# Kernel tuning notes

Hardware: AMD Instinct MI355X
Metric: run time of the kernel (lower is better)

## Reference

```python
import jax, jax.numpy as jnp
import numpy as np

B, T, D = 2, 2048, 1024
H, DH = 16, 64


def setup_inputs() -> dict:
    key = jax.random.key(0)
    ks = jax.random.split(key, 8)
    return {
        "x": jax.random.normal(ks[0], (B, T, D), dtype=jnp.float32),
        "mask": jnp.ones((1, 1, T, T), dtype=bool),
        "Wq": jax.random.normal(ks[1], (D, D), dtype=jnp.float32) * 0.02,
        "Wk": jax.random.normal(ks[2], (D, D), dtype=jnp.float32) * 0.02,
        "Wv": jax.random.normal(ks[3], (D, D), dtype=jnp.float32) * 0.02,
        "Wo": jax.random.normal(ks[4], (D, D), dtype=jnp.float32) * 0.02,
        "S_q": jax.random.normal(ks[5], (H, DH, DH), dtype=jnp.float32),
        "S_k": jax.random.normal(ks[6], (H, DH, DH), dtype=jnp.float32),
    }


def reference(x, mask, Wq, Wk, Wv, Wo, S_q, S_k):
    b, t, _ = x.shape
    scale = DH ** (-0.5)
    # nn.Linear applies x @ W.T; our Wq etc. are the Linear weight matrices.
    def split_heads(y):
        return y.reshape(b, t, H, DH).transpose(0, 2, 1, 3)  # (B,H,T,DH)

    Q = split_heads(x @ Wq.T)
    K = split_heads(x @ Wk.T)
    V = split_heads(x @ Wv.T)
    Qp = jnp.einsum('bhtd,hde->bhte', Q, S_q)
    Kp = jnp.einsum('bhtd,hde->bhte', K, S_k)
    scores = jnp.einsum('bhte,bhse->bhts', Qp, Kp) * scale  # (B,H,T,T)
    scores = jnp.where(mask, scores, -jnp.inf)
    attn = jax.nn.softmax(scores, axis=-1)
    out = jnp.einsum('bhts,bhsd->bhtd', attn, V)
    out = out.transpose(0, 2, 1, 3).reshape(b, t, D)
    return out @ Wo.T
```

## Files before the change

kernel.cpp:

```cpp
#include <hip/hip_runtime.h>
#include <cstdint>
#include <cmath>


#define B_   2
#define T_   2048
#define Dm   1024
#define H_   16
#define DH_  64
#define Ntok (B_ * T_)
#define ND   (Ntok * Dm)
#define DD   (Dm * Dm)
#define QKS  2048

typedef _Float16 f16;
typedef _Float16 f16x4 __attribute__((ext_vector_type(4)));
typedef _Float16 f16x8 __attribute__((ext_vector_type(8)));
typedef float    f32x4 __attribute__((ext_vector_type(4)));

__device__ inline f32x4 mfma16(f16x8 a, f16x8 b, f32x4 c) {
  return __builtin_amdgcn_mfma_f32_16x16x32_f16(a, b, c, 0, 0, 0);
}

__device__ inline void async16(const void* g, void* l) {
  __builtin_amdgcn_global_load_lds(
      (const __attribute__((address_space(1))) unsigned int*)g,
      (__attribute__((address_space(3))) unsigned int*)l, 16, 0, 0);
}

__device__ inline float vmax4(f32x4 v) {
  return fmaxf(fmaxf(v[0], v[1]), fmaxf(v[2], v[3]));
}
__device__ inline float vsum4(f32x4 v) {
  return (v[0] + v[1]) + (v[2] + v[3]);
}

__global__ void cvt_all(const float* __restrict__ x, const float* __restrict__ Wv,
                        const float* __restrict__ Wo, f16* __restrict__ x_f,
                        f16* __restrict__ WvDst, f16* __restrict__ Wo_f) {
  int i = (blockIdx.x * 256 + threadIdx.x) * 4;
  const float* src;
  f16* dst;
  int off;
  if (i < ND) {
    src = x; dst = x_f; off = i;
  } else if (i < ND + DD) {
    src = Wv; dst = WvDst; off = i - ND;
  } else {
    src = Wo; dst = Wo_f; off = i - ND - DD;
  }
  f32x4 v = *(const f32x4*)(src + off);
  f16x4 o;
#pragma unroll
  for (int j = 0; j < 4; ++j) o[j] = (f16)v[j];
  *(f16x4*)(dst + off) = o;
}

__global__ __launch_bounds__(64) void fold_w2(
    const float* __restrict__ Wq, const float* __restrict__ Sq,
    const float* __restrict__ Wk, const float* __restrict__ Sk,
    f16* __restrict__ T) {
  __shared__ __align__(16) float sS[64 * 64];
  const int tid = threadIdx.x;
  const int hy = blockIdx.y;
  const float* W = (hy < 16) ? Wq : Wk;
  const float* S = (hy < 16) ? Sq : Sk;
  f16* out = T + (size_t)((hy < 16) ? 0 : 1024) * Dm;
  const int h = hy & 15;
  const int d = blockIdx.x * 64 + tid;
#pragma unroll 8
  for (int i = 0; i < 64; ++i) sS[i * 64 + tid] = S[h * 4096 + i * 64 + tid];
  __syncthreads();
  float acc[64];
#pragma unroll
  for (int e = 0; e < 64; ++e) acc[e] = 0.f;
  for (int c = 0; c < 64; ++c) {
    float wv = W[(size_t)(h * 64 + c) * Dm + d];
    const f32x4* srow = (const f32x4*)&sS[c * 64];
#pragma unroll
    for (int e4 = 0; e4 < 16; ++e4) {
      f32x4 sv = srow[e4];
      acc[e4 * 4 + 0] += wv * sv[0];
      acc[e4 * 4 + 1] += wv * sv[1];
      acc[e4 * 4 + 2] += wv * sv[2];
      acc[e4 * 4 + 3] += wv * sv[3];
    }
  }
#pragma unroll
  for (int e = 0; e < 64; ++e)
    out[(size_t)(h * 64 + e) * Dm + d] = (f16)acc[e];
}

template <int OUTMODE, int TN>
__global__ __launch_bounds__(256) void gemm_bt(
    const f16* __restrict__ A, const f16* __restrict__ B,
    float* __restrict__ Cf, f16* __restrict__ Ch, f16* __restrict__ Ct,
    int M, int N, int K) {
  constexpr int AS = 128 * 32;
  constexpr int BS = TN * 32;
  constexpr int MT = (TN == 128) ? 4 : 2;
  extern __shared__ __align__(16) f16 smem[];

  const int tid = threadIdx.x;
  const int w = tid >> 6, lane = tid & 63, g = lane >> 4, ln = lane & 15;
  const int wm = (TN == 128) ? (w >> 1) * 64 : w * 32;
  const int wn = (TN == 128) ? (w & 1) * 64 : 0;
  const int bm = blockIdx.y * 128, bn = blockIdx.x * TN;

  f32x4 acc[MT][4] = {};
  const int r0 = tid >> 2;
  const int kb = (tid & 3) * 8;

  auto issue = [&](int kc, int buf) {
    f16* dA = smem + buf * AS;
    f16* dB = smem + 2 * AS + buf * BS;
#pragma unroll
    for (int i = 0; i < 2; ++i) {
      size_t aoff = (size_t)(bm + i * 64 + r0) * K + kc + kb;
      int lo = i * 4096 + w * 1024;
      async16(A + aoff, (char*)dA + lo);
      if (TN == 128 || i == 0) {
        size_t boff = (size_t)(bn + i * 64 + r0) * K + kc + kb;
        async16(B + boff, (char*)dB + lo);
      }
    }
  };

  issue(0, 0);
  const int KI = K / 32;
  for (int i = 0; i < KI; ++i) {
    __syncthreads();
    if (i + 1 < KI) issue((i + 1) * 32, (i + 1) & 1);
    const f16* cA = smem + (i & 1) * AS;
    const f16* cB = smem + 2 * AS + (i & 1) * BS;
    f16x8 af[MT];
#pragma unroll
    for (int mt = 0; mt < MT; ++mt)
      af[mt] = *(const f16x8*)&cA[(wm + mt * 16 + ln) * 32 + g * 8];
#pragma unroll
    for (int nt = 0; nt < 4; ++nt) {
      f16x8 bf = *(const f16x8*)&cB[(wn + nt * 16 + ln) * 32 + g * 8];
#pragma unroll
      for (int mt = 0; mt < MT; ++mt)
        acc[mt][nt] = mfma16(af[mt], bf, acc[mt][nt]);
    }
  }

  if (OUTMODE == 3 && bn >= 2048) {
#pragma unroll
    for (int mt = 0; mt < MT; ++mt)
#pragma unroll
      for (int nt = 0; nt < 4; ++nt) {
        int ch = bn - 2048 + wn + nt * 16 + ln;
        size_t base = (size_t)ch * Ntok + bm + wm + mt * 16 + g * 4;
        f16x4 ov;
#pragma unroll
        for (int r = 0; r < 4; ++r) ov[r] = (f16)acc[mt][nt][r];
        *(f16x4*)&Ct[base] = ov;
      }
    return;
  }
#pragma unroll
  for (int mt = 0; mt < MT; ++mt)
#pragma unroll
    for (int nt = 0; nt < 4; ++nt)
#pragma unroll
      for (int r = 0; r < 4; ++r) {
        int row = bm + wm + mt * 16 + g * 4 + r;
        int col = bn + wn + nt * 16 + ln;
        float v = acc[mt][nt][r];
        if (OUTMODE == 0) {
          Cf[(size_t)row * N + col] = v;
        } else {
          Ch[(size_t)row * QKS + col] = (f16)v;
        }
      }
}

__global__ __launch_bounds__(512) void flash_attn(
    const f16* __restrict__ QK, const f16* __restrict__ Vt,
    f16* __restrict__ O) {
  __shared__ __align__(16) f16 sKV[2 * 8192];
  __shared__ __align__(16) f16 sP[8 * 16 * 88];
  constexpr int VOFF = 4096;

  const int tid = threadIdx.x;
  const int w = tid >> 6, lane = tid & 63, g = lane >> 4, ln = lane & 15;
  const int bh = blockIdx.y, b = bh >> 4, h = bh & 15;
  const int q0 = blockIdx.x * 256 + w * 32;
  const size_t rowBase = (size_t)b * T_;
  const int hc = h * DH_;

  f16x8 qf[2][2];
#pragma unroll
  for (int t = 0; t < 2; ++t) {
    size_t qrow = (rowBase + q0 + t * 16 + ln) * (size_t)QKS + hc;
#pragma unroll
    for (int s = 0; s < 2; ++s)
      qf[t][s] = *(const f16x8*)(QK + qrow + s * 32 + g * 8);
  }

  float mrow[2] = {-INFINITY, -INFINITY}, lrow[2] = {0.f, 0.f};
  f32x4 oacc[2][4] = {};

  const int srow = tid >> 3;
  const int sel = ((tid & 7) * 8) ^ ((srow & 7) * 8);

  auto issue = [&](int kc, int buf) {
    char* base = (char*)sKV + buf * 16384;
    size_t koff = (rowBase + kc + srow) * (size_t)QKS + 1024 + hc + sel;
    async16(QK + koff, base + tid * 16);
    size_t voff = (size_t)(hc + srow) * Ntok + rowBase + kc + sel;
    async16(Vt + voff, base + 8192 + tid * 16);
  };

  issue(0, 0);
  constexpr int NC = T_ / 64;
  for (int i = 0; i < NC; ++i) {
    __syncthreads();
    if (i + 1 < NC) issue((i + 1) * 64, (i + 1) & 1);
    const f16* cK = sKV + (i & 1) * 8192;
    const f16* cVT = cK + VOFF;

    const int c0 = (g * 8) ^ ((ln & 7) * 8);
    const int c1 = (32 + g * 8) ^ ((ln & 7) * 8);

    f32x4 s4[2][4];
#pragma unroll
    for (int nt = 0; nt < 4; ++nt) {
      int row = (nt * 16 + ln) * 64;
      f16x8 k80 = *(const f16x8*)&cK[row + c0];
      f16x8 k81 = *(const f16x8*)&cK[row + c1];
#pragma unroll
      for (int t = 0; t < 2; ++t) {
        f32x4 a = {};
        a = mfma16(k80, qf[t][0], a);
        a = mfma16(k81, qf[t][1], a);
        s4[t][nt] = a * 0.1803368801111244f;
      }
    }

    f16* pw = sP + w * (16 * 88);
    f16x8 pb[2][2];
#pragma unroll
    for (int t = 0; t < 2; ++t) {
      f32x4 m4 = s4[t][0];
#pragma unroll
      for (int nt = 1; nt < 4; ++nt) {
        m4[0] = fmaxf(m4[0], s4[t][nt][0]);
        m4[1] = fmaxf(m4[1], s4[t][nt][1]);
        m4[2] = fmaxf(m4[2], s4[t][nt][2]);
        m4[3] = fmaxf(m4[3], s4[t][nt][3]);
      }
      float mx = vmax4(m4);
      mx = fmaxf(mx, __shfl_xor(mx, 16, 64));
      mx = fmaxf(mx, __shfl_xor(mx, 32, 64));
      float mn = fmaxf(mrow[t], mx);
      float alpha = __builtin_amdgcn_exp2f(mrow[t] - mn);
      mrow[t] = mn;
      f32x4 p4[4];
      f16x4 pk[4];
#pragma unroll
      for (int nt = 0; nt < 4; ++nt)
#pragma unroll
        for (int r = 0; r < 4; ++r) {
          float pv = __builtin_amdgcn_exp2f(s4[t][nt][r] - mn);
          p4[nt][r] = pv;
          pk[nt][r] = (f16)pv;
        }
      f32x4 sv4 = (p4[0] + p4[1]) + (p4[2] + p4[3]);
      float sum = vsum4(sv4);
      sum += __shfl_xor(sum, 16, 64);
      sum += __shfl_xor(sum, 32, 64);
      lrow[t] = lrow[t] * alpha + sum;
      if (__any(alpha != 1.0f)) {
#pragma unroll
        for (int dt = 0; dt < 4; ++dt) oacc[t][dt] *= alpha;
      }
#pragma unroll
      for (int nt = 0; nt < 4; ++nt)
        *(f16x4*)&pw[ln * 88 + nt * 16 + g * 4] = pk[nt];
      asm volatile("" ::: "memory");
#pragma unroll
      for (int s = 0; s < 2; ++s)
        pb[t][s] = *(const f16x8*)&pw[ln * 88 + s * 32 + g * 8];
      asm volatile("" ::: "memory");
    }

#pragma unroll
    for (int s = 0; s < 2; ++s) {
      int col = (s == 0) ? c0 : c1;
#pragma unroll
      for (int dt = 0; dt < 4; ++dt) {
        f16x8 va = *(const f16x8*)&cVT[(dt * 16 + ln) * 64 + col];
        oacc[0][dt] = mfma16(va, pb[0][s], oacc[0][dt]);
        oacc[1][dt] = mfma16(va, pb[1][s], oacc[1][dt]);
      }
    }
  }

#pragma unroll
  for (int t = 0; t < 2; ++t) {
    float rl = 1.0f / lrow[t];
    size_t orow = (rowBase + q0 + t * 16 + ln) * (size_t)Dm + hc;
#pragma unroll
    for (int dt = 0; dt < 4; ++dt) {
      f16x4 ov;
#pragma unroll
      for (int r = 0; r < 4; ++r) ov[r] = (f16)(oacc[t][dt][r] * rl);
      *(f16x4*)&O[orow + dt * 16 + g * 4] = ov;
    }
  }
}

extern "C" void kernel_launch(void* const* d_in, const int* in_sizes, int n_in,
                              void* d_out, int out_size, void* d_ws, size_t ws_size,
                              hipStream_t stream) {
  const float* x  = (const float*)d_in[0];
  const float* Wq = (const float*)d_in[2];
  const float* Wk = (const float*)d_in[3];
  const float* Wv = (const float*)d_in[4];
  const float* Wo = (const float*)d_in[5];
  const float* Sq = (const float*)d_in[6];
  const float* Sk = (const float*)d_in[7];

  char* p = (char*)d_ws;
  auto alloc = [&](size_t bytes) {
    char* r = p;
    p += (bytes + 255) & ~(size_t)255;
    return r;
  };
  f16* x_f   = (f16*)alloc((size_t)ND * 2);
  f16* Wqkv  = (f16*)alloc((size_t)3 * DD * 2);
  f16* Wo_f  = (f16*)alloc((size_t)DD * 2);
  f16* QK    = (f16*)alloc((size_t)Ntok * QKS * 2);
  f16* Vt_f  = (f16*)alloc((size_t)ND * 2);
  f16* AO    = (f16*)alloc((size_t)ND * 2);

  cvt_all<<<(ND + 2 * DD) / 1024, 256, 0, stream>>>(
      x, Wv, Wo, x_f, Wqkv + (size_t)2048 * Dm, Wo_f);
  fold_w2<<<dim3(16, 32), 64, 0, stream>>>(Wq, Sq, Wk, Sk, Wqkv);

  gemm_bt<3, 128><<<dim3(3072 / 128, Ntok / 128), 256, 32768, stream>>>(
      x_f, Wqkv, nullptr, QK, Vt_f, Ntok, 3072, Dm);

  flash_attn<<<dim3(T_ / 256, B_ * H_), 512, 0, stream>>>(QK, Vt_f, AO);

  gemm_bt<0, 64><<<dim3(Dm / 64, Ntok / 128), 256, 24576, stream>>>(
      AO, Wo_f, (float*)d_out, nullptr, nullptr, Ntok, Dm, Dm);
}
```

Before: 236.9 us.

## Split flash attention over two KV halves and merge with combine kernel

```diff
diff --git a/kernel.cpp b/kernel.cpp
--- a/kernel.cpp
+++ b/kernel.cpp
@@ -179,7 +179,7 @@
 
 __global__ __launch_bounds__(512) void flash_attn(
     const f16* __restrict__ QK, const f16* __restrict__ Vt,
-    f16* __restrict__ O) {
+    f16* __restrict__ Op, float* __restrict__ Mp, float* __restrict__ Lp) {
   __shared__ __align__(16) f16 sKV[2 * 8192];
   __shared__ __align__(16) f16 sP[8 * 16 * 88];
   constexpr int VOFF = 4096;
@@ -187,6 +187,8 @@
   const int tid = threadIdx.x;
   const int w = tid >> 6, lane = tid & 63, g = lane >> 4, ln = lane & 15;
   const int bh = blockIdx.y, b = bh >> 4, h = bh & 15;
+  const int sp = blockIdx.z;
+  const int kbase = sp * (T_ / 2);
   const int q0 = blockIdx.x * 256 + w * 32;
   const size_t rowBase = (size_t)b * T_;
   const int hc = h * DH_;
@@ -196,8 +198,12 @@
   for (int t = 0; t < 2; ++t) {
     size_t qrow = (rowBase + q0 + t * 16 + ln) * (size_t)QKS + hc;
 #pragma unroll
-    for (int s = 0; s < 2; ++s)
-      qf[t][s] = *(const f16x8*)(QK + qrow + s * 32 + g * 8);
+    for (int s = 0; s < 2; ++s) {
+      f16x8 q = *(const f16x8*)(QK + qrow + s * 32 + g * 8);
+#pragma unroll
+      for (int j = 0; j < 8; ++j) q[j] *= (f16)0.1803368801111244f;
+      qf[t][s] = q;
+    }
   }
 
   float mrow[2] = {-INFINITY, -INFINITY}, lrow[2] = {0.f, 0.f};
@@ -214,11 +220,11 @@
     async16(Vt + voff, base + 8192 + tid * 16);
   };
 
-  issue(0, 0);
-  constexpr int NC = T_ / 64;
+  issue(kbase, 0);
+  constexpr int NC = T_ / 2 / 64;
   for (int i = 0; i < NC; ++i) {
     __syncthreads();
-    if (i + 1 < NC) issue((i + 1) * 64, (i + 1) & 1);
+    if (i + 1 < NC) issue(kbase + (i + 1) * 64, (i + 1) & 1);
     const f16* cK = sKV + (i & 1) * 8192;
     const f16* cVT = cK + VOFF;
 
@@ -236,7 +242,7 @@
         f32x4 a = {};
         a = mfma16(k80, qf[t][0], a);
         a = mfma16(k81, qf[t][1], a);
-        s4[t][nt] = a * 0.1803368801111244f;
+        s4[t][nt] = a;
       }
     }
 
@@ -301,16 +307,47 @@
 
 #pragma unroll
   for (int t = 0; t < 2; ++t) {
-    float rl = 1.0f / lrow[t];
-    size_t orow = (rowBase + q0 + t * 16 + ln) * (size_t)Dm + hc;
+    size_t q = rowBase + q0 + t * 16 + ln;
+    size_t orow = ((size_t)sp * Ntok + q) * Dm + hc;
 #pragma unroll
     for (int dt = 0; dt < 4; ++dt) {
       f16x4 ov;
 #pragma unroll
-      for (int r = 0; r < 4; ++r) ov[r] = (f16)(oacc[t][dt][r] * rl);
-      *(f16x4*)&O[orow + dt * 16 + g * 4] = ov;
-    }
-  }
+      for (int r = 0; r < 4; ++r) ov[r] = (f16)oacc[t][dt][r];
+      *(f16x4*)&Op[orow + dt * 16 + g * 4] = ov;
+    }
+    if (g == 0) {
+      Mp[((size_t)sp * Ntok + q) * H_ + h] = mrow[t];
+      Lp[((size_t)sp * Ntok + q) * H_ + h] = lrow[t];
+    }
+  }
+}
+
+__global__ void flash_combine(const f16* __restrict__ Op,
+                              const float* __restrict__ Mp,
+                              const float* __restrict__ Lp,
+                              f16* __restrict__ AO) {
+  int idx = blockIdx.x * 256 + threadIdx.x;
+  int tok = idx >> 8;
+  int c4 = idx & 255;
+  int ch = c4 * 4;
+  int h = ch >> 6;
+  float m0 = Mp[(size_t)tok * H_ + h];
+  float m1 = Mp[((size_t)Ntok + tok) * H_ + h];
+  float l0 = Lp[(size_t)tok * H_ + h];
+  float l1 = Lp[((size_t)Ntok + tok) * H_ + h];
+  float mM = fmaxf(m0, m1);
+  float a0 = __builtin_amdgcn_exp2f(m0 - mM);
+  float a1 = __builtin_amdgcn_exp2f(m1 - mM);
+  float rl = 1.0f / (a0 * l0 + a1 * l1);
+  a0 *= rl;
+  a1 *= rl;
+  f16x4 o0 = *(const f16x4*)&Op[(size_t)tok * Dm + ch];
+  f16x4 o1 = *(const f16x4*)&Op[((size_t)Ntok + tok) * Dm + ch];
+  f16x4 ov;
+#pragma unroll
+  for (int r = 0; r < 4; ++r) ov[r] = (f16)(a0 * (float)o0[r] + a1 * (float)o1[r]);
+  *(f16x4*)&AO[(size_t)tok * Dm + ch] = ov;
 }
 
 extern "C" void kernel_launch(void* const* d_in, const int* in_sizes, int n_in,
@@ -330,12 +367,15 @@
     p += (bytes + 255) & ~(size_t)255;
     return r;
   };
-  f16* x_f   = (f16*)alloc((size_t)ND * 2);
-  f16* Wqkv  = (f16*)alloc((size_t)3 * DD * 2);
-  f16* Wo_f  = (f16*)alloc((size_t)DD * 2);
-  f16* QK    = (f16*)alloc((size_t)Ntok * QKS * 2);
-  f16* Vt_f  = (f16*)alloc((size_t)ND * 2);
-  f16* AO    = (f16*)alloc((size_t)ND * 2);
+  f16*   x_f  = (f16*)alloc((size_t)ND * 2);
+  f16*   Wqkv = (f16*)alloc((size_t)3 * DD * 2);
+  f16*   Wo_f = (f16*)alloc((size_t)DD * 2);
+  f16*   QK   = (f16*)alloc((size_t)Ntok * QKS * 2);
+  f16*   Vt_f = (f16*)alloc((size_t)ND * 2);
+  f16*   AO   = (f16*)alloc((size_t)ND * 2);
+  f16*   Op   = (f16*)alloc((size_t)2 * ND * 2);
+  float* Mp   = (float*)alloc((size_t)2 * Ntok * H_ * 4);
+  float* Lp   = (float*)alloc((size_t)2 * Ntok * H_ * 4);
 
   cvt_all<<<(ND + 2 * DD) / 1024, 256, 0, stream>>>(
       x, Wv, Wo, x_f, Wqkv + (size_t)2048 * Dm, Wo_f);
@@ -344,7 +384,9 @@
   gemm_bt<3, 128><<<dim3(3072 / 128, Ntok / 128), 256, 32768, stream>>>(
       x_f, Wqkv, nullptr, QK, Vt_f, Ntok, 3072, Dm);
 
-  flash_attn<<<dim3(T_ / 256, B_ * H_), 512, 0, stream>>>(QK, Vt_f, AO);
+  flash_attn<<<dim3(T_ / 256, B_ * H_, 2), 512, 0, stream>>>(QK, Vt_f,
+                                                             Op, Mp, Lp);
+  flash_combine<<<ND / 1024, 256, 0, stream>>>(Op, Mp, Lp, AO);
 
   gemm_bt<0, 64><<<dim3(Dm / 64, Ntok / 128), 256, 24576, stream>>>(
       AO, Wo_f, (float*)d_out, nullptr, nullptr, Ntok, Dm, Dm);
```

Result: faster. 227.1 us (-4.2%).
